# Kernel optimization log

Hardware: AMD Instinct MI355X
Metric: run time of the kernel (lower is better)

The kernel has to match this reference:

```python
import jax, jax.numpy as jnp
import numpy as np

T, B, I, H, RW, RU = 512, 64, 512, 512, 64, 64
WINIT = 0.1


def setup_inputs() -> dict:
    key = jax.random.key(0)
    ks = jax.random.split(key, 12)
    u = lambda k, shape: jax.random.uniform(k, shape, jnp.float32, -WINIT, WINIT)
    return {
        "x": jax.random.normal(ks[0], (T, B, I), jnp.float32),
        "h0": jnp.zeros((B, H), jnp.float32),
        "c0": jnp.zeros((B, H), jnp.float32),
        "U_x": u(ks[1], (I, RW)),
        "U_h": u(ks[2], (H, RU)),
        "W_x": u(ks[3], (4 * H, RW)),
        "W_h": u(ks[4], (4 * H, RU)),
        "b_x": u(ks[5], (4 * H,)),
        "b_h": u(ks[6], (4 * H,)),
        "dia_x": u(ks[7], (1, I)),
        "dia_h": u(ks[8], (1, H)),
    }


def reference(x, h0, c0, U_x, U_h, W_x, W_h, b_x, b_h, dia_x, dia_h):
    Tn, Bn, In = x.shape
    Hn = h0.shape[1]
    # Per-gate diagonal correction: sum_r U[:,r] * W[gate_slice, r] -> [4, H]
    Dx = jnp.sum(U_x[None, :, :] * W_x.reshape(4, Hn, -1), axis=-1)  # (I == H)
    Dh = jnp.sum(U_h[None, :, :] * W_h.reshape(4, Hn, -1), axis=-1)
    # Pre-batch all x-side gate pre-activations across time: [T, B, 4H]
    vm_x = jnp.tile(dia_x * x, (1, 1, 4))
    lowered_x = jnp.einsum("tbi,ir,gr->tbg", x, U_x, W_x)
    refined_x = (x[:, :, None, :] * Dx).reshape(Tn, Bn, 4 * Hn)
    gx_all = vm_x + lowered_x - refined_x + b_x

    def step(carry, gx):
        h, c = carry
        vm_h = jnp.tile(dia_h * h, (1, 4))
        lowered_h = (h @ U_h) @ W_h.T
        refined_h = (h[:, None, :] * Dh).reshape(Bn, 4 * Hn)
        g = gx + vm_h + lowered_h - refined_h + b_h
        xi, xf, xo, xn = jnp.split(g, 4, axis=1)
        i = jax.nn.sigmoid(xi)
        f = jax.nn.sigmoid(xf)
        o = jax.nn.sigmoid(xo)
        n = jnp.tanh(xn)
        c = f * c + i * n
        h = o * jnp.tanh(c)
        return (h, c), h

    (h, c), outputs = jax.lax.scan(step, (h0, c0), gx_all)
    return outputs, (h, c)
```

## Files before the change

kernel.cpp:

```cpp
#include <hip/hip_runtime.h>


typedef __fp16 h2f __attribute__((ext_vector_type(2)));
typedef unsigned int u32;
typedef unsigned short u16;

__device__ __forceinline__ float dot2f(u32 a, u32 b, float c) {
#if __has_builtin(__builtin_amdgcn_fdot2)
  return __builtin_amdgcn_fdot2(__builtin_bit_cast(h2f, a),
                                __builtin_bit_cast(h2f, b), c, false);
#else
  h2f x = __builtin_bit_cast(h2f, a);
  h2f y = __builtin_bit_cast(h2f, b);
  return c + (float)x[0] * (float)y[0] + (float)x[1] * (float)y[1];
#endif
}

__device__ __forceinline__ u32 pk2(float a, float b) {
#if __has_builtin(__builtin_amdgcn_cvt_pkrtz)
  return __builtin_bit_cast(u32, __builtin_amdgcn_cvt_pkrtz(a, b));
#else
  h2f h;
  h[0] = (__fp16)a;
  h[1] = (__fp16)b;
  return __builtin_bit_cast(u32, h);
#endif
}

__device__ __forceinline__ float h2f1(u16 u) {
  return (float)__builtin_bit_cast(__fp16, u);
}
__device__ __forceinline__ u16 f2h(float f) {
  return __builtin_bit_cast(u16, (__fp16)f);
}

__global__ void k0_prep(const float* __restrict__ Wx, const float* __restrict__ Wh,
                        const float* __restrict__ Ux, const float* __restrict__ Uh,
                        u32* __restrict__ WxP, u32* __restrict__ WhP,
                        u32* __restrict__ UxP, u32* __restrict__ UhP,
                        float* __restrict__ Dx, float* __restrict__ Dh) {
  int idx = blockIdx.x * 256 + threadIdx.x;
  if (idx < 65536) {
    WxP[idx] = pk2(Wx[2 * idx], Wx[2 * idx + 1]);
    WhP[idx] = pk2(Wh[2 * idx], Wh[2 * idx + 1]);
  }
  if (idx < 16384) {
    int r = idx >> 8, k2 = idx & 255;
    UxP[idx] = pk2(Ux[(2 * k2) * 64 + r], Ux[(2 * k2 + 1) * 64 + r]);
    UhP[idx] = pk2(Uh[(2 * k2) * 64 + r], Uh[(2 * k2 + 1) * 64 + r]);
  }
  if (idx < 4096) {
    int which = idx >> 11;
    int j = idx & 2047;
    int h = j & 511;
    const float* U = which ? Uh : Ux;
    const float* W = which ? Wh : Wx;
    float s = 0.f;
    for (int r = 0; r < 64; r++) s += U[h * 64 + r] * W[j * 64 + r];
    (which ? Dh : Dx)[j] = s;
  }
}

__global__ __launch_bounds__(256) void k1_xu(const float* __restrict__ x,
                                             const u32* __restrict__ UxP,
                                             u32* __restrict__ xuP) {
  __shared__ alignas(16) u32 xh[8192];
  const int tid = threadIdx.x;
  const int row0 = blockIdx.x * 32;
  const float* xs = x + (size_t)row0 * 512;

#pragma unroll
  for (int i = 0; i < 16; i++) {
    int f = tid + i * 256;
    float4 v = ((const float4*)xs)[f];
    xh[f * 2] = pk2(v.x, v.y);
    xh[f * 2 + 1] = pk2(v.z, v.w);
  }
  __syncthreads();

  const int w = tid >> 6, r = tid & 63;
  const int wr0 = w * 8;
  float acc[8] = {0.f, 0.f, 0.f, 0.f, 0.f, 0.f, 0.f, 0.f};
  const u32* Ubase = UxP + r * 256;

  for (int kc = 0; kc < 32; kc++) {
    uint4 u0 = *(const uint4*)(Ubase + kc * 8);
    uint4 u1 = *(const uint4*)(Ubase + kc * 8 + 4);
#pragma unroll
    for (int row = 0; row < 8; row++) {
      const uint4* xp = (const uint4*)&xh[(wr0 + row) * 256 + kc * 8];
      uint4 a0 = xp[0], a1 = xp[1];
      float a = acc[row];
      a = dot2f(a0.x, u0.x, a);
      a = dot2f(a0.y, u0.y, a);
      a = dot2f(a0.z, u0.z, a);
      a = dot2f(a0.w, u0.w, a);
      a = dot2f(a1.x, u1.x, a);
      a = dot2f(a1.y, u1.y, a);
      a = dot2f(a1.z, u1.z, a);
      a = dot2f(a1.w, u1.w, a);
      acc[row] = a;
    }
  }
#pragma unroll
  for (int row = 0; row < 8; row++) {
    float other = __shfl_xor(acc[row], 1, 64);
    if ((r & 1) == 0) {
      xuP[(size_t)(row0 + wr0 + row) * 32 + (r >> 1)] = pk2(acc[row], other);
    }
  }
}

__global__ __launch_bounds__(512, 2) void k2_gx(
    const float* __restrict__ x, const u32* __restrict__ xuP,
    const u32* __restrict__ WxP, const float* __restrict__ Dx,
    const float* __restrict__ bx, const float* __restrict__ diax,
    u16* __restrict__ gx) {
  __shared__ alignas(16) u32 xup[512];
  const int t = threadIdx.x;
  const int rows0 = blockIdx.x * 16;

  uint4 Wp[4][8];
#pragma unroll
  for (int g = 0; g < 4; g++) {
    const uint4* p = (const uint4*)(WxP + (size_t)(g * 512 + t) * 32);
#pragma unroll
    for (int m = 0; m < 8; m++) Wp[g][m] = p[m];
  }
  const float dia = diax[t];
  float Dg[4], bg[4];
#pragma unroll
  for (int g = 0; g < 4; g++) {
    Dg[g] = Dx[g * 512 + t];
    bg[g] = bx[g * 512 + t];
  }
  xup[t] = xuP[(size_t)rows0 * 32 + t];
  __syncthreads();

  for (int row = 0; row < 16; row++) {
    const uint4* xp = (const uint4*)&xup[row * 32];
    uint4 a[8];
#pragma unroll
    for (int m = 0; m < 8; m++) a[m] = xp[m];
    float xv = x[(size_t)(rows0 + row) * 512 + t];
    u16* gout = gx + (size_t)(rows0 + row) * 2048 + t;
#pragma unroll
    for (int g = 0; g < 4; g++) {
      float acc = 0.f;
#pragma unroll
      for (int m = 0; m < 8; m++) {
        acc = dot2f(a[m].x, Wp[g][m].x, acc);
        acc = dot2f(a[m].y, Wp[g][m].y, acc);
        acc = dot2f(a[m].z, Wp[g][m].z, acc);
        acc = dot2f(a[m].w, Wp[g][m].w, acc);
      }
      float pre = acc + xv * (dia - Dg[g]) + bg[g];
      gout[g * 512] = f2h(pre);
    }
  }
}

__global__ __launch_bounds__(512, 2) void k3_rnn(
    const u16* __restrict__ gx, const u32* __restrict__ WhP,
    const u32* __restrict__ UhP, const float* __restrict__ Dh,
    const float* __restrict__ bh, const float* __restrict__ diah,
    float* __restrict__ out) {
  __shared__ alignas(16) u16 h16[512];
  __shared__ float partial[512];
  __shared__ alignas(16) u16 hu16[64];

  const int t = threadIdx.x;
  const int b = blockIdx.x;

  uint4 Wp[4][8];
#pragma unroll
  for (int g = 0; g < 4; g++) {
    const uint4* p = (const uint4*)(WhP + (size_t)(g * 512 + t) * 32);
#pragma unroll
    for (int m = 0; m < 8; m++) Wp[g][m] = p[m];
  }
  uint4 Up[8];
  {
    const uint4* p = (const uint4*)(UhP + (size_t)(t & 63) * 256 + (t >> 6) * 32);
#pragma unroll
    for (int m = 0; m < 8; m++) Up[m] = p[m];
  }
  const float dia = diah[t];
  float Dg[4], bg[4];
#pragma unroll
  for (int g = 0; g < 4; g++) {
    Dg[g] = Dh[g * 512 + t];
    bg[g] = bh[g * 512 + t];
  }

  float h = 0.f, c = 0.f;
  h16[t] = 0;
  __syncthreads();

  const u16* gxb = gx + (size_t)b * 2048 + t;
  float* outb = out + (size_t)b * 512 + t;

  for (int ts = 0; ts < 512; ts++) {
    const u16* gp = gxb + (size_t)ts * (64 * 2048);
    float gxl[4];
#pragma unroll
    for (int g = 0; g < 4; g++) gxl[g] = h2f1(gp[g * 512]);

    float acc = 0.f;
    const uint4* hp = ((const uint4*)h16) + (t >> 6) * 8;
#pragma unroll
    for (int m = 0; m < 8; m++) {
      uint4 hv = hp[m];
      acc = dot2f(hv.x, Up[m].x, acc);
      acc = dot2f(hv.y, Up[m].y, acc);
      acc = dot2f(hv.z, Up[m].z, acc);
      acc = dot2f(hv.w, Up[m].w, acc);
    }
    partial[t] = acc;
    __syncthreads();
    if (t < 64) {
      float s = 0.f;
#pragma unroll
      for (int cc = 0; cc < 8; cc++) s += partial[cc * 64 + t];
      hu16[t] = f2h(s);
    }
    __syncthreads();

    uint4 hq[8];
    {
      const uint4* hup = (const uint4*)hu16;
#pragma unroll
      for (int m = 0; m < 8; m++) hq[m] = hup[m];
    }
    float pre[4];
#pragma unroll
    for (int g = 0; g < 4; g++) {
      float a2 = 0.f;
#pragma unroll
      for (int m = 0; m < 8; m++) {
        a2 = dot2f(hq[m].x, Wp[g][m].x, a2);
        a2 = dot2f(hq[m].y, Wp[g][m].y, a2);
        a2 = dot2f(hq[m].z, Wp[g][m].z, a2);
        a2 = dot2f(hq[m].w, Wp[g][m].w, a2);
      }
      pre[g] = a2 + gxl[g] + h * (dia - Dg[g]) + bg[g];
    }
    float ig = 1.f / (1.f + __expf(-pre[0]));
    float fg = 1.f / (1.f + __expf(-pre[1]));
    float og = 1.f / (1.f + __expf(-pre[2]));
    float e2 = __expf(2.f * pre[3]);
    float ng = 1.f - 2.f / (e2 + 1.f);
    c = fg * c + ig * ng;
    float e2c = __expf(2.f * c);
    h = og * (1.f - 2.f / (e2c + 1.f));

    outb[(size_t)ts * 32768] = h;
    h16[t] = f2h(h);
    __syncthreads();
  }
  out[(size_t)512 * 32768 + (size_t)b * 512 + t] = h;
  out[(size_t)512 * 32768 + 32768 + (size_t)b * 512 + t] = c;
}

extern "C" void kernel_launch(void* const* d_in, const int* in_sizes, int n_in,
                              void* d_out, int out_size, void* d_ws,
                              size_t ws_size, hipStream_t stream) {
  const float* x = (const float*)d_in[0];
  const float* Ux = (const float*)d_in[3];
  const float* Uh = (const float*)d_in[4];
  const float* Wx = (const float*)d_in[5];
  const float* Wh = (const float*)d_in[6];
  const float* bx = (const float*)d_in[7];
  const float* bh = (const float*)d_in[8];
  const float* diax = (const float*)d_in[9];
  const float* diah = (const float*)d_in[10];
  float* out = (float*)d_out;

  char* ws = (char*)d_ws;
  u16* gx = (u16*)ws;
  u32* xuP = (u32*)(ws + 134217728);
  u32* WxP = (u32*)(ws + 138412032);
  u32* WhP = (u32*)(ws + 138674176);
  u32* UxP = (u32*)(ws + 138936320);
  u32* UhP = (u32*)(ws + 139001856);
  float* Dx = (float*)(ws + 139067392);
  float* Dh = (float*)(ws + 139075584);

  k0_prep<<<256, 256, 0, stream>>>(Wx, Wh, Ux, Uh, WxP, WhP, UxP, UhP, Dx, Dh);
  k1_xu<<<1024, 256, 0, stream>>>(x, UxP, xuP);
  k2_gx<<<2048, 512, 0, stream>>>(x, xuP, WxP, Dx, bx, diax, gx);
  k3_rnn<<<64, 512, 0, stream>>>(gx, WhP, UhP, Dh, bh, diah, out);
}
```

Baseline: 958.8 us.

## Split RNN step across 1024 threads, prefetch gx, interleave gate layout

The recurrent kernel now uses 1024 threads per batch row. Each half computes half of the rank-64 W_h dot product, and the partial sums are combined through shared memory. The U_h reduction moves to a transposed shared layout with shuffles, and the next timestep's gx values are prefetched so the global load is off the critical path. The gx precompute kernel processes 64 rows per block with interleaved gate outputs stored as ushort4. The change adds an extra barrier per step and leaves half the threads idle during the gate nonlinearities.

```diff
diff --git a/kernel.cpp b/kernel.cpp
--- a/kernel.cpp
+++ b/kernel.cpp
@@ -116,9 +116,9 @@
     const u32* __restrict__ WxP, const float* __restrict__ Dx,
     const float* __restrict__ bx, const float* __restrict__ diax,
     u16* __restrict__ gx) {
-  __shared__ alignas(16) u32 xup[512];
+  __shared__ alignas(16) u32 xus[2048];
   const int t = threadIdx.x;
-  const int rows0 = blockIdx.x * 16;
+  const int rows0 = blockIdx.x * 64;
 
   uint4 Wp[4][8];
 #pragma unroll
@@ -134,132 +134,164 @@
     Dg[g] = Dx[g * 512 + t];
     bg[g] = bx[g * 512 + t];
   }
-  xup[t] = xuP[(size_t)rows0 * 32 + t];
+#pragma unroll
+  for (int i = 0; i < 4; i++) xus[t + i * 512] = xuP[(size_t)rows0 * 32 + t + i * 512];
   __syncthreads();
 
-  for (int row = 0; row < 16; row++) {
-    const uint4* xp = (const uint4*)&xup[row * 32];
-    uint4 a[8];
-#pragma unroll
-    for (int m = 0; m < 8; m++) a[m] = xp[m];
-    float xv = x[(size_t)(rows0 + row) * 512 + t];
-    u16* gout = gx + (size_t)(rows0 + row) * 2048 + t;
-#pragma unroll
-    for (int g = 0; g < 4; g++) {
-      float acc = 0.f;
-#pragma unroll
-      for (int m = 0; m < 8; m++) {
-        acc = dot2f(a[m].x, Wp[g][m].x, acc);
-        acc = dot2f(a[m].y, Wp[g][m].y, acc);
-        acc = dot2f(a[m].z, Wp[g][m].z, acc);
-        acc = dot2f(a[m].w, Wp[g][m].w, acc);
-      }
-      float pre = acc + xv * (dia - Dg[g]) + bg[g];
-      gout[g * 512] = f2h(pre);
-    }
-  }
-}
-
-__global__ __launch_bounds__(512, 2) void k3_rnn(
+  ushort4* gx4 = (ushort4*)gx;
+  for (int row = 0; row < 64; row++) {
+    const int R = rows0 + row;
+    const uint4* s = (const uint4*)(xus + row * 32);
+    float xv = x[(size_t)R * 512 + t];
+    float a0 = 0.f, a1 = 0.f, a2 = 0.f, a3 = 0.f;
+#pragma unroll
+    for (int m = 0; m < 8; m++) {
+      uint4 sm = s[m];
+      uint4 w0 = Wp[0][m], w1 = Wp[1][m], w2 = Wp[2][m], w3 = Wp[3][m];
+      a0 = dot2f(sm.x, w0.x, a0); a0 = dot2f(sm.y, w0.y, a0);
+      a0 = dot2f(sm.z, w0.z, a0); a0 = dot2f(sm.w, w0.w, a0);
+      a1 = dot2f(sm.x, w1.x, a1); a1 = dot2f(sm.y, w1.y, a1);
+      a1 = dot2f(sm.z, w1.z, a1); a1 = dot2f(sm.w, w1.w, a1);
+      a2 = dot2f(sm.x, w2.x, a2); a2 = dot2f(sm.y, w2.y, a2);
+      a2 = dot2f(sm.z, w2.z, a2); a2 = dot2f(sm.w, w2.w, a2);
+      a3 = dot2f(sm.x, w3.x, a3); a3 = dot2f(sm.y, w3.y, a3);
+      a3 = dot2f(sm.z, w3.z, a3); a3 = dot2f(sm.w, w3.w, a3);
+    }
+    ushort4 o;
+    o.x = f2h(a0 + xv * (dia - Dg[0]) + bg[0]);
+    o.y = f2h(a1 + xv * (dia - Dg[1]) + bg[1]);
+    o.z = f2h(a2 + xv * (dia - Dg[2]) + bg[2]);
+    o.w = f2h(a3 + xv * (dia - Dg[3]) + bg[3]);
+    gx4[(size_t)R * 512 + t] = o;
+  }
+}
+
+__global__ __launch_bounds__(1024) void k3_rnn(
     const u16* __restrict__ gx, const u32* __restrict__ WhP,
     const u32* __restrict__ UhP, const float* __restrict__ Dh,
     const float* __restrict__ bh, const float* __restrict__ diah,
     float* __restrict__ out) {
-  __shared__ alignas(16) u16 h16[512];
-  __shared__ float partial[512];
-  __shared__ alignas(16) u16 hu16[64];
+  __shared__ alignas(16) u32 h32[256];
+  __shared__ float partial[16 * 68];
+  __shared__ alignas(16) u32 hu32[32];
+  __shared__ alignas(16) float4 preB[512];
 
   const int t = threadIdx.x;
   const int b = blockIdx.x;
-
-  uint4 Wp[4][8];
+  const int lane = t & 63;
+  const int w = t >> 6;
+  const int j = t & 511;
+  const int half = t >> 9;
+
+  uint4 Wp[4][4];
 #pragma unroll
   for (int g = 0; g < 4; g++) {
-    const uint4* p = (const uint4*)(WhP + (size_t)(g * 512 + t) * 32);
-#pragma unroll
-    for (int m = 0; m < 8; m++) Wp[g][m] = p[m];
-  }
-  uint4 Up[8];
+    const uint4* p = (const uint4*)(WhP + (size_t)(g * 512 + j) * 32 + half * 16);
+#pragma unroll
+    for (int m = 0; m < 4; m++) Wp[g][m] = p[m];
+  }
+  uint4 Up[4];
   {
-    const uint4* p = (const uint4*)(UhP + (size_t)(t & 63) * 256 + (t >> 6) * 32);
-#pragma unroll
-    for (int m = 0; m < 8; m++) Up[m] = p[m];
-  }
-  const float dia = diah[t];
-  float Dg[4], bg[4];
-#pragma unroll
-  for (int g = 0; g < 4; g++) {
-    Dg[g] = Dh[g * 512 + t];
-    bg[g] = bh[g * 512 + t];
+    const uint4* p = (const uint4*)(UhP + lane * 256 + w * 16);
+#pragma unroll
+    for (int m = 0; m < 4; m++) Up[m] = p[m];
+  }
+  float dia = 0.f, Dg[4] = {0.f, 0.f, 0.f, 0.f}, bg[4] = {0.f, 0.f, 0.f, 0.f};
+  if (half == 0) {
+    dia = diah[j];
+#pragma unroll
+    for (int g = 0; g < 4; g++) {
+      Dg[g] = Dh[g * 512 + j];
+      bg[g] = bh[g * 512 + j];
+    }
   }
 
   float h = 0.f, c = 0.f;
-  h16[t] = 0;
+  if (t < 256) h32[t] = 0u;
   __syncthreads();
 
-  const u16* gxb = gx + (size_t)b * 2048 + t;
-  float* outb = out + (size_t)b * 512 + t;
+  const ushort4* gx4 = (const ushort4*)gx;
+  const size_t gbase = (size_t)b * 512 + j;
+  float* outb = out + (size_t)b * 512 + j;
+
+  ushort4 gcur = {0, 0, 0, 0};
+  if (half == 0) gcur = gx4[gbase];
 
   for (int ts = 0; ts < 512; ts++) {
-    const u16* gp = gxb + (size_t)ts * (64 * 2048);
-    float gxl[4];
-#pragma unroll
-    for (int g = 0; g < 4; g++) gxl[g] = h2f1(gp[g * 512]);
-
+    ushort4 gnext = gcur;
+    if (half == 0) {
+      int tn = ts + (ts < 511);
+      gnext = gx4[(size_t)tn * 32768 + gbase];
+    }
+
+    const uint4* hp = ((const uint4*)h32) + w * 4;
     float acc = 0.f;
-    const uint4* hp = ((const uint4*)h16) + (t >> 6) * 8;
-#pragma unroll
-    for (int m = 0; m < 8; m++) {
+#pragma unroll
+    for (int m = 0; m < 4; m++) {
       uint4 hv = hp[m];
-      acc = dot2f(hv.x, Up[m].x, acc);
-      acc = dot2f(hv.y, Up[m].y, acc);
-      acc = dot2f(hv.z, Up[m].z, acc);
-      acc = dot2f(hv.w, Up[m].w, acc);
-    }
-    partial[t] = acc;
+      uint4 uq = Up[m];
+      acc = dot2f(hv.x, uq.x, acc);
+      acc = dot2f(hv.y, uq.y, acc);
+      acc = dot2f(hv.z, uq.z, acc);
+      acc = dot2f(hv.w, uq.w, acc);
+    }
+    partial[w * 68 + lane] = acc;
     __syncthreads();
-    if (t < 64) {
-      float s = 0.f;
-#pragma unroll
-      for (int cc = 0; cc < 8; cc++) s += partial[cc * 64 + t];
-      hu16[t] = f2h(s);
-    }
+
+    float pv = partial[(t & 15) * 68 + (t >> 4)];
+    pv += __shfl_xor(pv, 1);
+    pv += __shfl_xor(pv, 2);
+    pv += __shfl_xor(pv, 4);
+    pv += __shfl_xor(pv, 8);
+    float qv = __shfl_xor(pv, 16);
+    if ((lane & 31) == 0) hu32[2 * w + (lane >> 5)] = pk2(pv, qv);
     __syncthreads();
 
-    uint4 hq[8];
-    {
-      const uint4* hup = (const uint4*)hu16;
-#pragma unroll
-      for (int m = 0; m < 8; m++) hq[m] = hup[m];
-    }
-    float pre[4];
-#pragma unroll
-    for (int g = 0; g < 4; g++) {
-      float a2 = 0.f;
-#pragma unroll
-      for (int m = 0; m < 8; m++) {
-        a2 = dot2f(hq[m].x, Wp[g][m].x, a2);
-        a2 = dot2f(hq[m].y, Wp[g][m].y, a2);
-        a2 = dot2f(hq[m].z, Wp[g][m].z, a2);
-        a2 = dot2f(hq[m].w, Wp[g][m].w, a2);
-      }
-      pre[g] = a2 + gxl[g] + h * (dia - Dg[g]) + bg[g];
-    }
-    float ig = 1.f / (1.f + __expf(-pre[0]));
-    float fg = 1.f / (1.f + __expf(-pre[1]));
-    float og = 1.f / (1.f + __expf(-pre[2]));
-    float e2 = __expf(2.f * pre[3]);
-    float ng = 1.f - 2.f / (e2 + 1.f);
-    c = fg * c + ig * ng;
-    float e2c = __expf(2.f * c);
-    h = og * (1.f - 2.f / (e2c + 1.f));
-
-    outb[(size_t)ts * 32768] = h;
-    h16[t] = f2h(h);
+    const uint4* hup = ((const uint4*)hu32) + half * 4;
+    float a0 = 0.f, a1 = 0.f, a2 = 0.f, a3 = 0.f;
+#pragma unroll
+    for (int m = 0; m < 4; m++) {
+      uint4 hm = hup[m];
+      uint4 w0 = Wp[0][m], w1 = Wp[1][m], w2 = Wp[2][m], w3 = Wp[3][m];
+      a0 = dot2f(hm.x, w0.x, a0); a0 = dot2f(hm.y, w0.y, a0);
+      a0 = dot2f(hm.z, w0.z, a0); a0 = dot2f(hm.w, w0.w, a0);
+      a1 = dot2f(hm.x, w1.x, a1); a1 = dot2f(hm.y, w1.y, a1);
+      a1 = dot2f(hm.z, w1.z, a1); a1 = dot2f(hm.w, w1.w, a1);
+      a2 = dot2f(hm.x, w2.x, a2); a2 = dot2f(hm.y, w2.y, a2);
+      a2 = dot2f(hm.z, w2.z, a2); a2 = dot2f(hm.w, w2.w, a2);
+      a3 = dot2f(hm.x, w3.x, a3); a3 = dot2f(hm.y, w3.y, a3);
+      a3 = dot2f(hm.z, w3.z, a3); a3 = dot2f(hm.w, w3.w, a3);
+    }
+    if (half == 1) {
+      float4 v; v.x = a0; v.y = a1; v.z = a2; v.w = a3;
+      preB[j] = v;
+    }
     __syncthreads();
-  }
-  out[(size_t)512 * 32768 + (size_t)b * 512 + t] = h;
-  out[(size_t)512 * 32768 + 32768 + (size_t)b * 512 + t] = c;
+
+    if (half == 0) {
+      float4 pb = preB[j];
+      float pre0 = a0 + pb.x + h2f1(gcur.x) + h * (dia - Dg[0]) + bg[0];
+      float pre1 = a1 + pb.y + h2f1(gcur.y) + h * (dia - Dg[1]) + bg[1];
+      float pre2 = a2 + pb.z + h2f1(gcur.z) + h * (dia - Dg[2]) + bg[2];
+      float pre3 = a3 + pb.w + h2f1(gcur.w) + h * (dia - Dg[3]) + bg[3];
+      float ig = 1.f / (1.f + __expf(-pre0));
+      float fg = 1.f / (1.f + __expf(-pre1));
+      float og = 1.f / (1.f + __expf(-pre2));
+      float e2 = __expf(2.f * pre3);
+      float ng = 1.f - 2.f / (e2 + 1.f);
+      c = fg * c + ig * ng;
+      float e2c = __expf(2.f * c);
+      h = og * (1.f - 2.f / (e2c + 1.f));
+      outb[(size_t)ts * 32768] = h;
+      ((u16*)h32)[j] = f2h(h);
+    }
+    gcur = gnext;
+    __syncthreads();
+  }
+  if (half == 0) {
+    out[(size_t)512 * 32768 + (size_t)b * 512 + j] = h;
+    out[(size_t)512 * 32768 + 32768 + (size_t)b * 512 + j] = c;
+  }
 }
 
 extern "C" void kernel_launch(void* const* d_in, const int* in_sizes, int n_in,
@@ -288,6 +320,6 @@
 
   k0_prep<<<256, 256, 0, stream>>>(Wx, Wh, Ux, Uh, WxP, WhP, UxP, UhP, Dx, Dh);
   k1_xu<<<1024, 256, 0, stream>>>(x, UxP, xuP);
-  k2_gx<<<2048, 512, 0, stream>>>(x, xuP, WxP, Dx, bx, diax, gx);
-  k3_rnn<<<64, 512, 0, stream>>>(gx, WhP, UhP, Dh, bh, diah, out);
-}
+  k2_gx<<<512, 512, 0, stream>>>(x, xuP, WxP, Dx, bx, diax, gx);
+  k3_rnn<<<64, 1024, 0, stream>>>(gx, WhP, UhP, Dh, bh, diah, out);
+}
```

After: 1.084 ms. 1.13x slower.
